# Performance work log

Hardware: AMD Instinct MI355X
Metric: run time of the kernel (lower is better)

The kernel has to match this reference:

```python
import jax, jax.numpy as jnp
import numpy as np

TOPK_OUTER = 15  # hard-coded k in topk_loss
TOPK_INNER = 4   # self.topk


def avgpool2x2(x, t):
    # t applications of 2x2/stride-2 average pooling on NCHW
    for _ in range(t):
        B, C, H, W = x.shape
        x = x.reshape(B, C, H // 2, 2, W // 2, 2).mean(axis=(3, 5))
    return x


def flatten_chw(x):
    # NCHW -> [B*H*W, C]
    B, C, H, W = x.shape
    return jnp.transpose(x, (0, 2, 3, 1)).reshape(-1, C)


def cosine_similar(q, p):
    # inner product divided by outer product of L2 norms (as in source)
    inner = jnp.einsum('ik,sk->is', q, p)
    qn = jnp.sqrt(jnp.einsum('ik,ik->i', q, q))
    pn = jnp.sqrt(jnp.einsum('sk,sk->s', p, p))
    return inner / (qn[:, None] * pn[None, :])


def setup_inputs() -> dict:
    key = jax.random.key(0)
    kq, ks = jax.random.split(key)
    q = jax.random.normal(kq, (64, 512, 32, 32), dtype=jnp.float32)
    S = jax.random.normal(ks, (128, 512, 32, 32), dtype=jnp.float32)
    return {"q": q, "S": S}


def reference(q, S):
    C = S.shape[1]
    qf = flatten_chw(avgpool2x2(q, 2))                 # [Nq, C]
    s_src = flatten_chw(avgpool2x2(S, 2))              # [Ns2, C]
    s1 = flatten_chw(avgpool2x2(S, 1))                 # [Ns1, C]
    s_all = jnp.concatenate([s1, s_src], axis=0)       # [Ns, C]
    sim = cosine_similar(qf, s_all)                    # [Nq, Ns]
    q2s, _ = jax.lax.top_k(sim, TOPK_OUTER)            # [Nq, 15]
    probs = jax.nn.softmax(q2s, axis=-1)
    topk_v, _ = jax.lax.top_k(probs, TOPK_INNER)       # [Nq, 4]
    loss = -jnp.log(topk_v).mean(axis=-1).mean()
    return loss
```

## Files before the change

### kernel.cpp

```cpp
#include <hip/hip_runtime.h>
#include <hip/hip_bf16.h>
#include <stdint.h>

#define NQ 4096
#define NS 40960
#define CDIM 512
#define QT 256
#define SC 32
#define NSPLIT 32
#define SPER (NS / NSPLIT)
#define NCHUNK (SPER / SC)
#define NCAND 960

typedef float f32x16 __attribute__((ext_vector_type(16)));
typedef unsigned int u32x4 __attribute__((ext_vector_type(4)));
typedef int i32x4 __attribute__((ext_vector_type(4)));
typedef int i32x8 __attribute__((ext_vector_type(8)));

__device__ __forceinline__ unsigned short f2bf(float f) {
    uint32_t u = __builtin_bit_cast(uint32_t, f);
    u += 0x7fffu + ((u >> 16) & 1u);
    return (unsigned short)(u >> 16);
}
__device__ __forceinline__ float bf2f(unsigned short u) {
    uint32_t x = ((uint32_t)u) << 16;
    return __builtin_bit_cast(float, x);
}

__device__ __forceinline__ unsigned fp4enc(float y) {
    float m = fabsf(y);
    unsigned c = (m < 0.25f) ? 0u : (m < 0.75f) ? 1u : (m < 1.25f) ? 2u
               : (m < 1.75f) ? 3u : (m < 2.5f)  ? 4u : (m < 3.5f)  ? 5u
               : (m < 5.0f)  ? 6u : 7u;
    return c | ((__builtin_bit_cast(unsigned, y) >> 28) & 8u);
}

__device__ __forceinline__ void async_load16(const void* g, void* l) {
    auto gp = reinterpret_cast<const __attribute__((address_space(1))) uint32_t*>(
        reinterpret_cast<uintptr_t>(g));
    auto lp = reinterpret_cast<__attribute__((address_space(3))) uint32_t*>(
        reinterpret_cast<uintptr_t>(l));
    __builtin_amdgcn_global_load_lds(gp, lp, 16 , 0, 0);
}

__device__ __forceinline__ void ins15(float (&r)[15], float v) {
#pragma unroll
    for (int i = 14; i >= 1; --i) r[i] = __builtin_amdgcn_fmed3f(v, r[i - 1], r[i]);
    r[0] = fmaxf(r[0], v);
}

__global__ __launch_bounds__(256) void pool_q_norm(const float* __restrict__ q,
                                                   unsigned char* __restrict__ qn) {
    int bb = blockIdx.x >> 3, h = blockIdx.x & 7;
    int t = threadIdx.x, lane = t & 63, wid = t >> 6;
    float vals[2][8];
    float ss[8] = {0, 0, 0, 0, 0, 0, 0, 0};
#pragma unroll
    for (int e = 0; e < 2; ++e) {
        int c = 2 * t + e;
        const float* base = q + ((size_t)(bb * 512 + c) * 1024 + 4 * h * 32);
#pragma unroll
        for (int w2 = 0; w2 < 8; ++w2) vals[e][w2] = 0.f;
#pragma unroll
        for (int i = 0; i < 4; ++i) {
            const float4* row = (const float4*)(base + i * 32);
#pragma unroll
            for (int w2 = 0; w2 < 8; ++w2) {
                float4 v = row[w2];
                vals[e][w2] += (v.x + v.y) + (v.z + v.w);
            }
        }
#pragma unroll
        for (int w2 = 0; w2 < 8; ++w2) {
            vals[e][w2] *= (1.f / 16.f);
            ss[w2] += vals[e][w2] * vals[e][w2];
        }
    }
    __shared__ float red[8][4];
#pragma unroll
    for (int k = 0; k < 8; ++k) {
        float v = ss[k];
#pragma unroll
        for (int o = 32; o > 0; o >>= 1) v += __shfl_xor(v, o, 64);
        if (lane == 0) red[k][wid] = v;
    }
    __syncthreads();
#pragma unroll
    for (int w2 = 0; w2 < 8; ++w2) {
        float inv16 = rsqrtf(red[w2][0] + red[w2][1] + red[w2][2] + red[w2][3]) * 16.f;
        unsigned e0 = fp4enc(vals[0][w2] * inv16);
        unsigned e1 = fp4enc(vals[1][w2] * inv16);
        qn[(size_t)(bb * 64 + h * 8 + w2) * 256 + t] = (unsigned char)(e0 | (e1 << 4));
    }
}

__global__ __launch_bounds__(256) void pool_s_norm(const float* __restrict__ S,
                                                   unsigned char* __restrict__ sn) {
    int bb = blockIdx.x >> 3, h2 = blockIdx.x & 7;
    int t = threadIdx.x, lane = t & 63, wid = t >> 6;
    __shared__ unsigned short tile[40 * 512];
    __shared__ float rowsum[40];
#pragma unroll
    for (int e = 0; e < 2; ++e) {
        int c = 2 * t + e;
        const float* base = S + ((size_t)(bb * 512 + c) * 1024 + 4 * h2 * 32);
        float s1v[2][16];
#pragma unroll
        for (int j = 0; j < 2; ++j) {
            const float4* r0 = (const float4*)(base + (2 * j) * 32);
            const float4* r1 = (const float4*)(base + (2 * j + 1) * 32);
#pragma unroll
            for (int f = 0; f < 8; ++f) {
                float4 a = r0[f], b2 = r1[f];
                s1v[j][2 * f]     = (a.x + a.y + b2.x + b2.y) * 0.25f;
                s1v[j][2 * f + 1] = (a.z + a.w + b2.z + b2.w) * 0.25f;
            }
        }
#pragma unroll
        for (int j = 0; j < 2; ++j)
#pragma unroll
            for (int w1 = 0; w1 < 16; ++w1)
                tile[(j * 16 + w1) * 512 + c] = f2bf(s1v[j][w1]);
#pragma unroll
        for (int w2 = 0; w2 < 8; ++w2) {
            float src = (s1v[0][2 * w2] + s1v[0][2 * w2 + 1] +
                         s1v[1][2 * w2] + s1v[1][2 * w2 + 1]) * 0.25f;
            tile[(32 + w2) * 512 + c] = f2bf(src);
        }
    }
    __syncthreads();
#pragma unroll
    for (int k = 0; k < 10; ++k) {
        int row = 4 * k + wid;
        u32x4 d = *(const u32x4*)(&tile[row * 512 + lane * 8]);
        float s = 0.f;
#pragma unroll
        for (int j = 0; j < 4; ++j) {
            float x0 = bf2f((unsigned short)(d[j] & 0xffffu));
            float x1 = bf2f((unsigned short)(d[j] >> 16));
            s += x0 * x0 + x1 * x1;
        }
#pragma unroll
        for (int o = 32; o > 0; o >>= 1) s += __shfl_xor(s, o, 64);
        if (lane == 0) rowsum[row] = s;
    }
    __syncthreads();
#pragma unroll
    for (int k = 0; k < 10; ++k) {
        int idx = t + 256 * k;
        int r = idx >> 6, seg = idx & 63;
        float inv16 = rsqrtf(rowsum[r]) * 16.f;
        const unsigned short* src = &tile[r * 512 + seg * 8];
        unsigned out = 0;
#pragma unroll
        for (int m = 0; m < 8; ++m)
            out |= fp4enc(bf2f(src[m]) * inv16) << (4 * m);
        int grow = (r < 32) ? (bb * 256 + (2 * h2 + (r >> 4)) * 16 + (r & 15))
                            : (32768 + bb * 64 + h2 * 8 + (r - 32));
        *(unsigned*)(sn + (size_t)grow * 256 + seg * 4) = out;
    }
}

__global__ __launch_bounds__(256, 2) void sim_topk(const unsigned char* __restrict__ qn,
                                                   const unsigned char* __restrict__ sn,
                                                   float* __restrict__ partial) {
    __shared__ char Bs[3][SC * 256];
    int id = blockIdx.x;
    int xcd = id & 7, j = id >> 3;
    int y = xcd * 4 + (j & 3);
    int x = j >> 2;
    int tid = threadIdx.x, lane = tid & 63, wid = tid >> 6;
    int rlo = lane & 31, hi = lane >> 5;
    int qbase = x * QT + wid * 64;
    int sbase = y * SPER;
    char* BsB = &Bs[0][0];

    u32x4 b[2][8];
#pragma unroll
    for (int g = 0; g < 2; ++g) {
        const unsigned char* qp = qn + (size_t)(qbase + g * 32 + rlo) * 256 + hi * 16;
#pragma unroll
        for (int kk = 0; kk < 8; ++kk) b[g][kk] = *(const u32x4*)(qp + kk * 32);
    }

    float r0[15], r1[15];
#pragma unroll
    for (int i = 0; i < 15; ++i) { r0[i] = -2.0f; r1[i] = -2.0f; }

    auto stage = [&](int ch, int buf) {
#pragma unroll
        for (int ii = 0; ii < 2; ++ii) {
            int g = (wid * 2 + ii) * 64 + lane;
            int row = g >> 4, s = g & 15;
            size_t srcoff = (size_t)(sbase + ch * SC + row) * 256
                          + (size_t)((s ^ (row & 15)) << 4);
            async_load16(sn + srcoff, BsB + buf * 8192 + (g << 4));
        }
    };

    auto kstep = [&](const char* B0, int kk, f32x16& acc0, f32x16& acc1) {
        int s0 = kk * 2 + hi;
        u32x4 a4 = *(const u32x4*)(B0 + rlo * 256 + ((s0 ^ (rlo & 15)) << 4));
        i32x4 ai = __builtin_bit_cast(i32x4, a4);
        i32x8 a = __builtin_shufflevector(ai, (i32x4){0, 0, 0, 0}, 0, 1, 2, 3, 4, 5, 6, 7);
        i32x8 b0 = __builtin_shufflevector(__builtin_bit_cast(i32x4, b[0][kk]),
                                           (i32x4){0, 0, 0, 0}, 0, 1, 2, 3, 4, 5, 6, 7);
        i32x8 b1 = __builtin_shufflevector(__builtin_bit_cast(i32x4, b[1][kk]),
                                           (i32x4){0, 0, 0, 0}, 0, 1, 2, 3, 4, 5, 6, 7);
        acc0 = __builtin_amdgcn_mfma_scale_f32_32x32x64_f8f6f4(
            a, b0, acc0, 4, 4, 0, 0x7B7B7B7B, 0, 0x7B7B7B7B);
        acc1 = __builtin_amdgcn_mfma_scale_f32_32x32x64_f8f6f4(
            a, b1, acc1, 4, 4, 0, 0x7B7B7B7B, 0, 0x7B7B7B7B);
    };

    stage(0, 0);
    stage(1, 1);
    f32x16 cA0, cA1, pB0, pB1;
#pragma unroll
    for (int e = 0; e < 16; ++e) { pB0[e] = -2.0f; pB1[e] = -2.0f; }
    int bufR = 0, bufS = 2, chS = 2;

    for (int it = 0; it < NCHUNK / 2; ++it) {
        asm volatile("s_waitcnt vmcnt(2)" ::: "memory");
        __builtin_amdgcn_s_barrier();
        stage(chS, bufS);
        chS = (chS + 1 == NCHUNK) ? 0 : chS + 1;
        bufS = (bufS + 1 == 3) ? 0 : bufS + 1;
#pragma unroll
        for (int g = 0; g < 2; ++g)
#pragma unroll
            for (int kk = 0; kk < 8; ++kk) asm volatile("" : "+v"(b[g][kk]));
        const char* B0 = BsB + bufR * 8192;
        bufR = (bufR + 1 == 3) ? 0 : bufR + 1;
#pragma unroll
        for (int e = 0; e < 16; ++e) { cA0[e] = 0.f; cA1[e] = 0.f; }
#pragma unroll
        for (int kk = 0; kk < 8; ++kk) {
            kstep(B0, kk, cA0, cA1);
            ins15(r0, pB0[2 * kk]);
            ins15(r0, pB0[2 * kk + 1]);
            ins15(r1, pB1[2 * kk]);
            ins15(r1, pB1[2 * kk + 1]);
        }

        asm volatile("s_waitcnt vmcnt(2)" ::: "memory");
        __builtin_amdgcn_s_barrier();
        stage(chS, bufS);
        chS = (chS + 1 == NCHUNK) ? 0 : chS + 1;
        bufS = (bufS + 1 == 3) ? 0 : bufS + 1;
        const char* B1 = BsB + bufR * 8192;
        bufR = (bufR + 1 == 3) ? 0 : bufR + 1;
#pragma unroll
        for (int e = 0; e < 16; ++e) { pB0[e] = 0.f; pB1[e] = 0.f; }
#pragma unroll
        for (int kk = 0; kk < 8; ++kk) {
            kstep(B1, kk, pB0, pB1);
            ins15(r0, cA0[2 * kk]);
            ins15(r0, cA0[2 * kk + 1]);
            ins15(r1, cA1[2 * kk]);
            ins15(r1, cA1[2 * kk + 1]);
        }
    }
#pragma unroll
    for (int e = 0; e < 16; ++e) { ins15(r0, pB0[e]); ins15(r1, pB1[e]); }

    int q0 = qbase + rlo;
    float* dst0 = partial + (((size_t)q0 * NSPLIT + y) * 2 + hi) * 15;
    float* dst1 = partial + (((size_t)(q0 + 32) * NSPLIT + y) * 2 + hi) * 15;
#pragma unroll
    for (int i = 0; i < 15; ++i) { dst0[i] = r0[i]; dst1[i] = r1[i]; }
}

__global__ __launch_bounds__(256) void topk_loss(const float* __restrict__ partial,
                                                 float* __restrict__ accum) {
    int t = threadIdx.x, lane = t & 63, wid = t >> 6;
    int r = blockIdx.x * 4 + wid;
    const float* src = partial + (size_t)r * NCAND;
    float v[15];
#pragma unroll
    for (int i = 0; i < 15; ++i) v[i] = src[lane + 64 * i];
    float m0 = 0.f, sexp = 0.f, top4 = 0.f;
#pragma unroll
    for (int round = 0; round < 15; ++round) {
        float m = v[0];
        int mi = lane * 16;
#pragma unroll
        for (int i = 1; i < 15; ++i)
            if (v[i] > m) { m = v[i]; mi = lane * 16 + i; }
#pragma unroll
        for (int o = 32; o > 0; o >>= 1) {
            float om = __shfl_xor(m, o, 64);
            int oi = __shfl_xor(mi, o, 64);
            if (om > m || (om == m && oi < mi)) { m = om; mi = oi; }
        }
        int wl = mi >> 4, wi = mi & 15;
#pragma unroll
        for (int i = 0; i < 15; ++i)
            if (i == wi && wl == lane) v[i] = -1e30f;
        if (round == 0) m0 = m;
        sexp += expf(m - m0);
        if (round < 4) top4 += m;
    }
    float loss = m0 + logf(sexp) - 0.25f * top4;
    __shared__ float red[4];
    if (lane == 0) red[wid] = loss;
    __syncthreads();
    if (t == 0) atomicAdd(accum, red[0] + red[1] + red[2] + red[3]);
}

__global__ void finalize_out(const float* __restrict__ accum, float* __restrict__ out) {
    out[0] = accum[0] * (1.0f / (float)NQ);
}

extern "C" void kernel_launch(void* const* d_in, const int* in_sizes, int n_in,
                              void* d_out, int out_size, void* d_ws, size_t ws_size,
                              hipStream_t stream) {
    (void)in_sizes; (void)n_in; (void)out_size; (void)ws_size;
    const float* q = (const float*)d_in[0];
    const float* S = (const float*)d_in[1];
    char* ws = (char*)d_ws;
    unsigned char* qn = (unsigned char*)ws;
    unsigned char* sn = (unsigned char*)(ws + 1048576);
    float* partial = (float*)(ws + 1048576 + 10485760);
    float* accum   = (float*)(ws + 1048576 + 10485760 + 15728640);

    hipMemsetAsync(accum, 0, 4, stream);
    pool_q_norm<<<512, 256, 0, stream>>>(q, qn);
    pool_s_norm<<<1024, 256, 0, stream>>>(S, sn);
    sim_topk<<<512, 256, 0, stream>>>(qn, sn, partial);
    topk_loss<<<NQ / 4, 256, 0, stream>>>(partial, accum);
    finalize_out<<<1, 1, 0, stream>>>(accum, (float*)d_out);
}
```

Before: 264.2 us.

## Drop LDS staging in sim_topk and read S tiles directly per wave

Removes the triple-buffered global-to-LDS async staging of S chunks and the barriers around it. Each wave now loads its S fragments straight from global memory into registers. Each wave handles 32 query rows instead of 64, so the query tile shrinks to 128, the grid doubles to 1024 blocks, and the occupancy hint rises to 4 blocks per CU. This removes the barrier and LDS overhead but shares each S load across far fewer queries, so L1/L2 traffic rises and global load latency sits directly in the MFMA loop with no explicit prefetch.

New measurement: 312.2 us. 1.18x slower.

```diff
diff --git a/kernel.cpp b/kernel.cpp
--- a/kernel.cpp
+++ b/kernel.cpp
@@ -5,7 +5,7 @@
 #define NQ 4096
 #define NS 40960
 #define CDIM 512
-#define QT 256
+#define QT 128
 #define SC 32
 #define NSPLIT 32
 #define SPER (NS / NSPLIT)
@@ -35,14 +35,6 @@
     return c | ((__builtin_bit_cast(unsigned, y) >> 28) & 8u);
 }
 
-__device__ __forceinline__ void async_load16(const void* g, void* l) {
-    auto gp = reinterpret_cast<const __attribute__((address_space(1))) uint32_t*>(
-        reinterpret_cast<uintptr_t>(g));
-    auto lp = reinterpret_cast<__attribute__((address_space(3))) uint32_t*>(
-        reinterpret_cast<uintptr_t>(l));
-    __builtin_amdgcn_global_load_lds(gp, lp, 16 , 0, 0);
-}
-
 __device__ __forceinline__ void ins15(float (&r)[15], float v) {
 #pragma unroll
     for (int i = 14; i >= 1; --i) r[i] = __builtin_amdgcn_fmed3f(v, r[i - 1], r[i]);
@@ -161,114 +153,74 @@
     }
 }
 
-__global__ __launch_bounds__(256, 2) void sim_topk(const unsigned char* __restrict__ qn,
+__global__ __launch_bounds__(256, 4) void sim_topk(const unsigned char* __restrict__ qn,
                                                    const unsigned char* __restrict__ sn,
                                                    float* __restrict__ partial) {
-    __shared__ char Bs[3][SC * 256];
     int id = blockIdx.x;
     int xcd = id & 7, j = id >> 3;
     int y = xcd * 4 + (j & 3);
     int x = j >> 2;
     int tid = threadIdx.x, lane = tid & 63, wid = tid >> 6;
     int rlo = lane & 31, hi = lane >> 5;
-    int qbase = x * QT + wid * 64;
+    int qbase = x * QT + wid * 32;
     int sbase = y * SPER;
-    char* BsB = &Bs[0][0];
-
-    u32x4 b[2][8];
-#pragma unroll
-    for (int g = 0; g < 2; ++g) {
-        const unsigned char* qp = qn + (size_t)(qbase + g * 32 + rlo) * 256 + hi * 16;
-#pragma unroll
-        for (int kk = 0; kk < 8; ++kk) b[g][kk] = *(const u32x4*)(qp + kk * 32);
-    }
-
-    float r0[15], r1[15];
-#pragma unroll
-    for (int i = 0; i < 15; ++i) { r0[i] = -2.0f; r1[i] = -2.0f; }
-
-    auto stage = [&](int ch, int buf) {
-#pragma unroll
-        for (int ii = 0; ii < 2; ++ii) {
-            int g = (wid * 2 + ii) * 64 + lane;
-            int row = g >> 4, s = g & 15;
-            size_t srcoff = (size_t)(sbase + ch * SC + row) * 256
-                          + (size_t)((s ^ (row & 15)) << 4);
-            async_load16(sn + srcoff, BsB + buf * 8192 + (g << 4));
-        }
+
+    u32x4 b[8];
+    {
+        const unsigned char* qp = qn + (size_t)(qbase + rlo) * 256 + hi * 16;
+#pragma unroll
+        for (int kk = 0; kk < 8; ++kk) b[kk] = *(const u32x4*)(qp + kk * 32);
+    }
+
+    float r0[15];
+#pragma unroll
+    for (int i = 0; i < 15; ++i) r0[i] = -2.0f;
+
+    auto kstep = [&](const unsigned char* s0, int kk, f32x16& acc) {
+        u32x4 a4 = *(const u32x4*)(s0 + kk * 32);
+        i32x8 a = __builtin_shufflevector(__builtin_bit_cast(i32x4, a4),
+                                          (i32x4){0, 0, 0, 0}, 0, 1, 2, 3, 4, 5, 6, 7);
+        i32x8 bk = __builtin_shufflevector(__builtin_bit_cast(i32x4, b[kk]),
+                                           (i32x4){0, 0, 0, 0}, 0, 1, 2, 3, 4, 5, 6, 7);
+        acc = __builtin_amdgcn_mfma_scale_f32_32x32x64_f8f6f4(
+            a, bk, acc, 4, 4, 0, 0x7B7B7B7B, 0, 0x7B7B7B7B);
     };
 
-    auto kstep = [&](const char* B0, int kk, f32x16& acc0, f32x16& acc1) {
-        int s0 = kk * 2 + hi;
-        u32x4 a4 = *(const u32x4*)(B0 + rlo * 256 + ((s0 ^ (rlo & 15)) << 4));
-        i32x4 ai = __builtin_bit_cast(i32x4, a4);
-        i32x8 a = __builtin_shufflevector(ai, (i32x4){0, 0, 0, 0}, 0, 1, 2, 3, 4, 5, 6, 7);
-        i32x8 b0 = __builtin_shufflevector(__builtin_bit_cast(i32x4, b[0][kk]),
-                                           (i32x4){0, 0, 0, 0}, 0, 1, 2, 3, 4, 5, 6, 7);
-        i32x8 b1 = __builtin_shufflevector(__builtin_bit_cast(i32x4, b[1][kk]),
-                                           (i32x4){0, 0, 0, 0}, 0, 1, 2, 3, 4, 5, 6, 7);
-        acc0 = __builtin_amdgcn_mfma_scale_f32_32x32x64_f8f6f4(
-            a, b0, acc0, 4, 4, 0, 0x7B7B7B7B, 0, 0x7B7B7B7B);
-        acc1 = __builtin_amdgcn_mfma_scale_f32_32x32x64_f8f6f4(
-            a, b1, acc1, 4, 4, 0, 0x7B7B7B7B, 0, 0x7B7B7B7B);
-    };
-
-    stage(0, 0);
-    stage(1, 1);
-    f32x16 cA0, cA1, pB0, pB1;
-#pragma unroll
-    for (int e = 0; e < 16; ++e) { pB0[e] = -2.0f; pB1[e] = -2.0f; }
-    int bufR = 0, bufS = 2, chS = 2;
+    f32x16 cA, pB;
+#pragma unroll
+    for (int e = 0; e < 16; ++e) pB[e] = -2.0f;
+
+    const unsigned char* sp = sn + (size_t)(sbase + rlo) * 256 + hi * 16;
 
     for (int it = 0; it < NCHUNK / 2; ++it) {
-        asm volatile("s_waitcnt vmcnt(2)" ::: "memory");
-        __builtin_amdgcn_s_barrier();
-        stage(chS, bufS);
-        chS = (chS + 1 == NCHUNK) ? 0 : chS + 1;
-        bufS = (bufS + 1 == 3) ? 0 : bufS + 1;
-#pragma unroll
-        for (int g = 0; g < 2; ++g)
-#pragma unroll
-            for (int kk = 0; kk < 8; ++kk) asm volatile("" : "+v"(b[g][kk]));
-        const char* B0 = BsB + bufR * 8192;
-        bufR = (bufR + 1 == 3) ? 0 : bufR + 1;
-#pragma unroll
-        for (int e = 0; e < 16; ++e) { cA0[e] = 0.f; cA1[e] = 0.f; }
+#pragma unroll
+        for (int kk = 0; kk < 8; ++kk) asm volatile("" : "+v"(b[kk]));
+        const unsigned char* s0 = sp + (size_t)(2 * it) * SC * 256;
+#pragma unroll
+        for (int e = 0; e < 16; ++e) cA[e] = 0.f;
 #pragma unroll
         for (int kk = 0; kk < 8; ++kk) {
-            kstep(B0, kk, cA0, cA1);
-            ins15(r0, pB0[2 * kk]);
-            ins15(r0, pB0[2 * kk + 1]);
-            ins15(r1, pB1[2 * kk]);
-            ins15(r1, pB1[2 * kk + 1]);
-        }
-
-        asm volatile("s_waitcnt vmcnt(2)" ::: "memory");
-        __builtin_amdgcn_s_barrier();
-        stage(chS, bufS);
-        chS = (chS + 1 == NCHUNK) ? 0 : chS + 1;
-        bufS = (bufS + 1 == 3) ? 0 : bufS + 1;
-        const char* B1 = BsB + bufR * 8192;
-        bufR = (bufR + 1 == 3) ? 0 : bufR + 1;
-#pragma unroll
-        for (int e = 0; e < 16; ++e) { pB0[e] = 0.f; pB1[e] = 0.f; }
+            kstep(s0, kk, cA);
+            ins15(r0, pB[2 * kk]);
+            ins15(r0, pB[2 * kk + 1]);
+        }
+        const unsigned char* s1 = s0 + SC * 256;
+#pragma unroll
+        for (int e = 0; e < 16; ++e) pB[e] = 0.f;
 #pragma unroll
         for (int kk = 0; kk < 8; ++kk) {
-            kstep(B1, kk, pB0, pB1);
-            ins15(r0, cA0[2 * kk]);
-            ins15(r0, cA0[2 * kk + 1]);
-            ins15(r1, cA1[2 * kk]);
-            ins15(r1, cA1[2 * kk + 1]);
-        }
-    }
-#pragma unroll
-    for (int e = 0; e < 16; ++e) { ins15(r0, pB0[e]); ins15(r1, pB1[e]); }
+            kstep(s1, kk, pB);
+            ins15(r0, cA[2 * kk]);
+            ins15(r0, cA[2 * kk + 1]);
+        }
+    }
+#pragma unroll
+    for (int e = 0; e < 16; ++e) ins15(r0, pB[e]);
 
     int q0 = qbase + rlo;
-    float* dst0 = partial + (((size_t)q0 * NSPLIT + y) * 2 + hi) * 15;
-    float* dst1 = partial + (((size_t)(q0 + 32) * NSPLIT + y) * 2 + hi) * 15;
-#pragma unroll
-    for (int i = 0; i < 15; ++i) { dst0[i] = r0[i]; dst1[i] = r1[i]; }
+    float* dst = partial + (((size_t)q0 * NSPLIT + y) * 2 + hi) * 15;
+#pragma unroll
+    for (int i = 0; i < 15; ++i) dst[i] = r0[i];
 }
 
 __global__ __launch_bounds__(256) void topk_loss(const float* __restrict__ partial,
@@ -327,7 +279,7 @@
     hipMemsetAsync(accum, 0, 4, stream);
     pool_q_norm<<<512, 256, 0, stream>>>(q, qn);
     pool_s_norm<<<1024, 256, 0, stream>>>(S, sn);
-    sim_topk<<<512, 256, 0, stream>>>(qn, sn, partial);
+    sim_topk<<<1024, 256, 0, stream>>>(qn, sn, partial);
     topk_loss<<<NQ / 4, 256, 0, stream>>>(partial, accum);
     finalize_out<<<1, 1, 0, stream>>>(accum, (float*)d_out);
 }
```

## Load S fragments directly from global and keep pooled S in registers

Applied to the files above, without the earlier changes.

sim_topk no longer stages S chunks into LDS with async global_load_lds and barriers. Each wave now reads its MFMA A-fragments straight from global memory (L2) into registers just before use, which removes shared-memory traffic and block-level synchronisation. pool_s_norm drops the bf16 LDS tile and keeps the pooled values in registers, reducing row norms with shuffles, and the fp4 encode no longer goes through bf16 rounding. The risks are exposed global-load latency with no software prefetch, four waves each loading the same S data redundantly, and higher register pressure in both kernels.

Measured after the change: 293.8 us. 1.11x slower.

```diff
diff --git a/kernel.cpp b/kernel.cpp
--- a/kernel.cpp
+++ b/kernel.cpp
@@ -17,11 +17,6 @@
 typedef int i32x4 __attribute__((ext_vector_type(4)));
 typedef int i32x8 __attribute__((ext_vector_type(8)));
 
-__device__ __forceinline__ unsigned short f2bf(float f) {
-    uint32_t u = __builtin_bit_cast(uint32_t, f);
-    u += 0x7fffu + ((u >> 16) & 1u);
-    return (unsigned short)(u >> 16);
-}
 __device__ __forceinline__ float bf2f(unsigned short u) {
     uint32_t x = ((uint32_t)u) << 16;
     return __builtin_bit_cast(float, x);
@@ -35,18 +30,16 @@
     return c | ((__builtin_bit_cast(unsigned, y) >> 28) & 8u);
 }
 
-__device__ __forceinline__ void async_load16(const void* g, void* l) {
-    auto gp = reinterpret_cast<const __attribute__((address_space(1))) uint32_t*>(
-        reinterpret_cast<uintptr_t>(g));
-    auto lp = reinterpret_cast<__attribute__((address_space(3))) uint32_t*>(
-        reinterpret_cast<uintptr_t>(l));
-    __builtin_amdgcn_global_load_lds(gp, lp, 16 , 0, 0);
-}
-
 __device__ __forceinline__ void ins15(float (&r)[15], float v) {
 #pragma unroll
     for (int i = 14; i >= 1; --i) r[i] = __builtin_amdgcn_fmed3f(v, r[i - 1], r[i]);
     r[0] = fmaxf(r[0], v);
+}
+
+__device__ __forceinline__ i32x8 frag8(u32x4 v) {
+    return __builtin_shufflevector(__builtin_bit_cast(i32x4, v),
+                                   __builtin_bit_cast(i32x4, v),
+                                   0, 1, 2, 3, -1, -1, -1, -1);
 }
 
 __global__ __launch_bounds__(256) void pool_q_norm(const float* __restrict__ q,
@@ -94,17 +87,15 @@
     }
 }
 
-__global__ __launch_bounds__(256) void pool_s_norm(const float* __restrict__ S,
-                                                   unsigned char* __restrict__ sn) {
+__global__ __launch_bounds__(256, 2) void pool_s_norm(const float* __restrict__ S,
+                                                      unsigned char* __restrict__ sn) {
     int bb = blockIdx.x >> 3, h2 = blockIdx.x & 7;
     int t = threadIdx.x, lane = t & 63, wid = t >> 6;
-    __shared__ unsigned short tile[40 * 512];
-    __shared__ float rowsum[40];
+    float v[2][40];
 #pragma unroll
     for (int e = 0; e < 2; ++e) {
         int c = 2 * t + e;
         const float* base = S + ((size_t)(bb * 512 + c) * 1024 + 4 * h2 * 32);
-        float s1v[2][16];
 #pragma unroll
         for (int j = 0; j < 2; ++j) {
             const float4* r0 = (const float4*)(base + (2 * j) * 32);
@@ -112,59 +103,41 @@
 #pragma unroll
             for (int f = 0; f < 8; ++f) {
                 float4 a = r0[f], b2 = r1[f];
-                s1v[j][2 * f]     = (a.x + a.y + b2.x + b2.y) * 0.25f;
-                s1v[j][2 * f + 1] = (a.z + a.w + b2.z + b2.w) * 0.25f;
+                v[e][j * 16 + 2 * f]     = (a.x + a.y + b2.x + b2.y) * 0.25f;
+                v[e][j * 16 + 2 * f + 1] = (a.z + a.w + b2.z + b2.w) * 0.25f;
             }
         }
 #pragma unroll
-        for (int j = 0; j < 2; ++j)
-#pragma unroll
-            for (int w1 = 0; w1 < 16; ++w1)
-                tile[(j * 16 + w1) * 512 + c] = f2bf(s1v[j][w1]);
-#pragma unroll
-        for (int w2 = 0; w2 < 8; ++w2) {
-            float src = (s1v[0][2 * w2] + s1v[0][2 * w2 + 1] +
-                         s1v[1][2 * w2] + s1v[1][2 * w2 + 1]) * 0.25f;
-            tile[(32 + w2) * 512 + c] = f2bf(src);
-        }
-    }
-    __syncthreads();
-#pragma unroll
-    for (int k = 0; k < 10; ++k) {
-        int row = 4 * k + wid;
-        u32x4 d = *(const u32x4*)(&tile[row * 512 + lane * 8]);
-        float s = 0.f;
-#pragma unroll
-        for (int j = 0; j < 4; ++j) {
-            float x0 = bf2f((unsigned short)(d[j] & 0xffffu));
-            float x1 = bf2f((unsigned short)(d[j] >> 16));
-            s += x0 * x0 + x1 * x1;
-        }
-#pragma unroll
-        for (int o = 32; o > 0; o >>= 1) s += __shfl_xor(s, o, 64);
-        if (lane == 0) rowsum[row] = s;
-    }
-    __syncthreads();
-#pragma unroll
-    for (int k = 0; k < 10; ++k) {
-        int idx = t + 256 * k;
-        int r = idx >> 6, seg = idx & 63;
-        float inv16 = rsqrtf(rowsum[r]) * 16.f;
-        const unsigned short* src = &tile[r * 512 + seg * 8];
-        unsigned out = 0;
-#pragma unroll
-        for (int m = 0; m < 8; ++m)
-            out |= fp4enc(bf2f(src[m]) * inv16) << (4 * m);
+        for (int w2 = 0; w2 < 8; ++w2)
+            v[e][32 + w2] = (v[e][2 * w2] + v[e][2 * w2 + 1] +
+                             v[e][16 + 2 * w2] + v[e][16 + 2 * w2 + 1]) * 0.25f;
+    }
+    __shared__ float red[40][4];
+    __shared__ float inv16s[40];
+#pragma unroll
+    for (int r = 0; r < 40; ++r) {
+        float p = v[0][r] * v[0][r] + v[1][r] * v[1][r];
+#pragma unroll
+        for (int o = 32; o > 0; o >>= 1) p += __shfl_xor(p, o, 64);
+        if (lane == 0) red[r][wid] = p;
+    }
+    __syncthreads();
+    if (t < 40) inv16s[t] = rsqrtf(red[t][0] + red[t][1] + red[t][2] + red[t][3]) * 16.f;
+    __syncthreads();
+#pragma unroll
+    for (int r = 0; r < 40; ++r) {
+        float iv = inv16s[r];
+        unsigned e0 = fp4enc(v[0][r] * iv);
+        unsigned e1 = fp4enc(v[1][r] * iv);
         int grow = (r < 32) ? (bb * 256 + (2 * h2 + (r >> 4)) * 16 + (r & 15))
                             : (32768 + bb * 64 + h2 * 8 + (r - 32));
-        *(unsigned*)(sn + (size_t)grow * 256 + seg * 4) = out;
+        sn[(size_t)grow * 256 + t] = (unsigned char)(e0 | (e1 << 4));
     }
 }
 
 __global__ __launch_bounds__(256, 2) void sim_topk(const unsigned char* __restrict__ qn,
                                                    const unsigned char* __restrict__ sn,
                                                    float* __restrict__ partial) {
-    __shared__ char Bs[3][SC * 256];
     int id = blockIdx.x;
     int xcd = id & 7, j = id >> 3;
     int y = xcd * 4 + (j & 3);
@@ -173,7 +146,6 @@
     int rlo = lane & 31, hi = lane >> 5;
     int qbase = x * QT + wid * 64;
     int sbase = y * SPER;
-    char* BsB = &Bs[0][0];
 
     u32x4 b[2][8];
 #pragma unroll
@@ -187,74 +159,48 @@
 #pragma unroll
     for (int i = 0; i < 15; ++i) { r0[i] = -2.0f; r1[i] = -2.0f; }
 
-    auto stage = [&](int ch, int buf) {
-#pragma unroll
-        for (int ii = 0; ii < 2; ++ii) {
-            int g = (wid * 2 + ii) * 64 + lane;
-            int row = g >> 4, s = g & 15;
-            size_t srcoff = (size_t)(sbase + ch * SC + row) * 256
-                          + (size_t)((s ^ (row & 15)) << 4);
-            async_load16(sn + srcoff, BsB + buf * 8192 + (g << 4));
-        }
-    };
-
-    auto kstep = [&](const char* B0, int kk, f32x16& acc0, f32x16& acc1) {
-        int s0 = kk * 2 + hi;
-        u32x4 a4 = *(const u32x4*)(B0 + rlo * 256 + ((s0 ^ (rlo & 15)) << 4));
-        i32x4 ai = __builtin_bit_cast(i32x4, a4);
-        i32x8 a = __builtin_shufflevector(ai, (i32x4){0, 0, 0, 0}, 0, 1, 2, 3, 4, 5, 6, 7);
-        i32x8 b0 = __builtin_shufflevector(__builtin_bit_cast(i32x4, b[0][kk]),
-                                           (i32x4){0, 0, 0, 0}, 0, 1, 2, 3, 4, 5, 6, 7);
-        i32x8 b1 = __builtin_shufflevector(__builtin_bit_cast(i32x4, b[1][kk]),
-                                           (i32x4){0, 0, 0, 0}, 0, 1, 2, 3, 4, 5, 6, 7);
-        acc0 = __builtin_amdgcn_mfma_scale_f32_32x32x64_f8f6f4(
-            a, b0, acc0, 4, 4, 0, 0x7B7B7B7B, 0, 0x7B7B7B7B);
-        acc1 = __builtin_amdgcn_mfma_scale_f32_32x32x64_f8f6f4(
-            a, b1, acc1, 4, 4, 0, 0x7B7B7B7B, 0, 0x7B7B7B7B);
-    };
-
-    stage(0, 0);
-    stage(1, 1);
     f32x16 cA0, cA1, pB0, pB1;
 #pragma unroll
     for (int e = 0; e < 16; ++e) { pB0[e] = -2.0f; pB1[e] = -2.0f; }
-    int bufR = 0, bufS = 2, chS = 2;
+
+    const unsigned char* sp = sn + (size_t)(sbase + rlo) * 256 + hi * 16;
 
     for (int it = 0; it < NCHUNK / 2; ++it) {
-        asm volatile("s_waitcnt vmcnt(2)" ::: "memory");
-        __builtin_amdgcn_s_barrier();
-        stage(chS, bufS);
-        chS = (chS + 1 == NCHUNK) ? 0 : chS + 1;
-        bufS = (bufS + 1 == 3) ? 0 : bufS + 1;
 #pragma unroll
         for (int g = 0; g < 2; ++g)
 #pragma unroll
             for (int kk = 0; kk < 8; ++kk) asm volatile("" : "+v"(b[g][kk]));
-        const char* B0 = BsB + bufR * 8192;
-        bufR = (bufR + 1 == 3) ? 0 : bufR + 1;
+        const unsigned char* s0 = sp + (size_t)(2 * it) * SC * 256;
+        u32x4 a4[8];
+#pragma unroll
+        for (int kk = 0; kk < 8; ++kk) a4[kk] = *(const u32x4*)(s0 + kk * 32);
 #pragma unroll
         for (int e = 0; e < 16; ++e) { cA0[e] = 0.f; cA1[e] = 0.f; }
 #pragma unroll
         for (int kk = 0; kk < 8; ++kk) {
-            kstep(B0, kk, cA0, cA1);
+            i32x8 a = frag8(a4[kk]);
+            cA0 = __builtin_amdgcn_mfma_scale_f32_32x32x64_f8f6f4(
+                a, frag8(b[0][kk]), cA0, 4, 4, 0, 0x7B7B7B7B, 0, 0x7B7B7B7B);
+            cA1 = __builtin_amdgcn_mfma_scale_f32_32x32x64_f8f6f4(
+                a, frag8(b[1][kk]), cA1, 4, 4, 0, 0x7B7B7B7B, 0, 0x7B7B7B7B);
             ins15(r0, pB0[2 * kk]);
             ins15(r0, pB0[2 * kk + 1]);
             ins15(r1, pB1[2 * kk]);
             ins15(r1, pB1[2 * kk + 1]);
         }
-
-        asm volatile("s_waitcnt vmcnt(2)" ::: "memory");
-        __builtin_amdgcn_s_barrier();
-        stage(chS, bufS);
-        chS = (chS + 1 == NCHUNK) ? 0 : chS + 1;
-        bufS = (bufS + 1 == 3) ? 0 : bufS + 1;
-        const char* B1 = BsB + bufR * 8192;
-        bufR = (bufR + 1 == 3) ? 0 : bufR + 1;
+        const unsigned char* s1 = s0 + SC * 256;
+        u32x4 a5[8];
+#pragma unroll
+        for (int kk = 0; kk < 8; ++kk) a5[kk] = *(const u32x4*)(s1 + kk * 32);
 #pragma unroll
         for (int e = 0; e < 16; ++e) { pB0[e] = 0.f; pB1[e] = 0.f; }
 #pragma unroll
         for (int kk = 0; kk < 8; ++kk) {
-            kstep(B1, kk, pB0, pB1);
+            i32x8 a = frag8(a5[kk]);
+            pB0 = __builtin_amdgcn_mfma_scale_f32_32x32x64_f8f6f4(
+                a, frag8(b[0][kk]), pB0, 4, 4, 0, 0x7B7B7B7B, 0, 0x7B7B7B7B);
+            pB1 = __builtin_amdgcn_mfma_scale_f32_32x32x64_f8f6f4(
+                a, frag8(b[1][kk]), pB1, 4, 4, 0, 0x7B7B7B7B, 0, 0x7B7B7B7B);
             ins15(r0, cA0[2 * kk]);
             ins15(r0, cA0[2 * kk + 1]);
             ins15(r1, cA1[2 * kk]);
```
